# Kernel tuning notes

Measured on AMD Instinct MI355X. Metric: run time of the kernel, lower is better.

## Reference

```python
import jax, jax.numpy as jnp
import numpy as np

EMBED = 1024
HEADS = 16
HEAD_DIM = EMBED // HEADS
EPS = 1e-8


def setup_inputs() -> dict:
    key = jax.random.key(0)
    ks = jax.random.split(key, 10)
    s = 1.0 / np.sqrt(EMBED)
    return {
        "hidden_input": jax.random.normal(ks[0], (4, 2048, EMBED), dtype=jnp.float32),
        "Wq": jax.random.uniform(ks[1], (EMBED, EMBED), jnp.float32, -s, s),
        "bq": jax.random.uniform(ks[2], (EMBED,), jnp.float32, -s, s),
        "Wk": jax.random.uniform(ks[3], (EMBED, EMBED), jnp.float32, -s, s),
        "bk": jax.random.uniform(ks[4], (EMBED,), jnp.float32, -s, s),
        "Wv": jax.random.uniform(ks[5], (EMBED, EMBED), jnp.float32, -s, s),
        "bv": jax.random.uniform(ks[6], (EMBED,), jnp.float32, -s, s),
        "Wp": jax.random.uniform(ks[7], (EMBED, EMBED), jnp.float32, -s, s),
        "bp": jax.random.uniform(ks[8], (EMBED,), jnp.float32, -s, s),
        "gamma": jnp.ones((EMBED,), jnp.float32),
        "beta": jnp.zeros((EMBED,), jnp.float32),
    }


def reference(hidden_input, Wq, bq, Wk, bk, Wv, bv, Wp, bp, gamma, beta):
    n, l, e = hidden_input.shape
    h, d = HEADS, HEAD_DIM

    def split_heads(x):  # [n, l, e] -> [n, h, l, d]
        return x.reshape(n, l, h, d).transpose(0, 2, 1, 3)

    q = split_heads(hidden_input @ Wq + bq)
    k = split_heads(hidden_input @ Wk + bk)
    v = split_heads(hidden_input @ Wv + bv)

    scores = jnp.einsum("nhqd,nhkd->nhqk", q, k) / jnp.sqrt(jnp.float32(d))
    attn = jax.nn.softmax(scores, axis=-1)
    ctx = jnp.einsum("nhqk,nhkd->nhqd", attn, v)
    ctx = ctx.transpose(0, 2, 1, 3).reshape(n, l, e)

    out = ctx @ Wp + bp
    x = out + hidden_input
    mu = jnp.mean(x, axis=-1, keepdims=True)
    var = jnp.mean(jnp.square(x - mu), axis=-1, keepdims=True)
    return (x - mu) / jnp.sqrt(var + EPS) * gamma + beta
```

## Files before the change

### kernel.cpp

```cpp
#include <hip/hip_runtime.h>

#define EMBED 1024
#define SEQ   2048
#define BATCH 4
#define HEADS 16

typedef __attribute__((ext_vector_type(8))) short short8;
typedef __attribute__((ext_vector_type(4))) float floatx4;
typedef __attribute__((ext_vector_type(16))) float floatx16;

#define MFMA16(a, b, c) __builtin_amdgcn_mfma_f32_16x16x32_bf16((a), (b), (c), 0, 0, 0)
#define MFMA32(a, b, c) __builtin_amdgcn_mfma_f32_32x32x16_bf16((a), (b), (c), 0, 0, 0)
#define ATT_SCALE (0.125f * 1.44269504088896340736f)

static __device__ __forceinline__ unsigned short f2bf(float f) {
  union { float f; unsigned int u; } v; v.f = f;
  unsigned int u = v.u;
  u += 0x7fffu + ((u >> 16) & 1u);
  return (unsigned short)(u >> 16);
}

static __device__ __forceinline__ unsigned cvtpk(float lo, float hi) {
  unsigned r;
  asm("v_cvt_pk_bf16_f32 %0, %1, %2" : "=v"(r) : "v"(lo), "v"(hi));
  return r;
}

static __device__ __forceinline__ void async16(const unsigned short* g, unsigned short* l) {
  __builtin_amdgcn_global_load_lds(
      (const __attribute__((address_space(1))) void*)g,
      (__attribute__((address_space(3))) void*)l, 16, 0, 0);
}

__global__ __launch_bounds__(256) void k_prep(const float* __restrict__ hid,
                                              unsigned short* __restrict__ hidA,
                                              const float* __restrict__ Wq, const float* __restrict__ Wk,
                                              const float* __restrict__ Wv, const float* __restrict__ Wp,
                                              unsigned short* __restrict__ WT) {
  __shared__ unsigned short tile[64][65];
  const int bid = blockIdx.x, tid = threadIdx.x;
  if (bid < 4096) {
    int i = bid * 256 + tid;
    const float4* s = (const float4*)hid;
    float4 a = s[i * 2], b = s[i * 2 + 1];
    uint4 o;
    o.x = (unsigned)f2bf(a.x) | ((unsigned)f2bf(a.y) << 16);
    o.y = (unsigned)f2bf(a.z) | ((unsigned)f2bf(a.w) << 16);
    o.z = (unsigned)f2bf(b.x) | ((unsigned)f2bf(b.y) << 16);
    o.w = (unsigned)f2bf(b.z) | ((unsigned)f2bf(b.w) << 16);
    ((uint4*)hidA)[i] = o;
    return;
  }
  const int idx = bid - 4096;
  const int z = idx >> 8, rem = idx & 255;
  const float* src = (z == 0) ? Wq : (z == 1) ? Wk : (z == 2) ? Wv : Wp;
  unsigned short* dst = WT + (size_t)z * EMBED * EMBED;
  const int k0 = (rem & 15) * 64, n0 = (rem >> 4) * 64;
  for (int i = tid; i < 4096; i += 256) {
    int r = i >> 6, c = i & 63;
    tile[c][r] = f2bf(src[(size_t)(k0 + r) * EMBED + n0 + c]);
  }
  __syncthreads();
  for (int i = tid; i < 4096; i += 256) {
    int r = i >> 6, c = i & 63;
    dst[(size_t)(n0 + r) * EMBED + k0 + c] = tile[r][c];
  }
}

__global__ __launch_bounds__(256) void k_gemm_qkv(const unsigned short* __restrict__ A,
                                                  const unsigned short* __restrict__ BT,
                                                  const float* __restrict__ bq,
                                                  const float* __restrict__ bk,
                                                  const float* __restrict__ bv,
                                                  unsigned short* __restrict__ C,
                                                  unsigned short* __restrict__ VT) {
  __shared__ unsigned short Als[128 * 64];
  __shared__ unsigned short Bls[128 * 64];
  const int tid = threadIdx.x;
  const int by = blockIdx.y;
  const bool vmode = (by >= 16);
  const int arow0 = vmode ? (by - 16) * 128 : blockIdx.x * 128;
  const int brow0 = vmode ? blockIdx.x * 128 : by * 128;
  const int w = tid >> 6, lane = tid & 63, l16 = lane & 15, quad = lane >> 4;
  const int l7 = l16 & 7;
  const int wrow = (w >> 1) * 64, wcol = (w & 1) * 64;

  floatx4 acc[4][4];
#pragma unroll
  for (int i = 0; i < 4; ++i)
#pragma unroll
    for (int j = 0; j < 4; ++j) acc[i][j] = {0.f, 0.f, 0.f, 0.f};

  const int srow = tid >> 3;
  const int scol = (((tid & 7) ^ (srow & 7)) * 8);
  const unsigned short* Arow = vmode ? (BT + (size_t)2 * EMBED * EMBED) : A;
  const unsigned short* Brow = vmode ? A : BT;
  const unsigned short* Ap = Arow + (size_t)(arow0 + srow) * EMBED + scol;
  const unsigned short* Bp = Brow + (size_t)(brow0 + srow) * EMBED + scol;

  int ab[2], bb[2];
#pragma unroll
  for (int kc = 0; kc < 2; ++kc) {
    ab[kc] = (wrow + l16) * 64 + (((4 * kc + quad) ^ l7) << 3);
    bb[kc] = (wcol + l16) * 64 + (((4 * kc + quad) ^ l7) << 3);
  }

  for (int kt = 0; kt < 16; ++kt) {
    const int k0 = kt * 64;
#pragma unroll
    for (int i = 0; i < 4; ++i)
      async16(Ap + k0 + (size_t)i * 32 * EMBED, Als + i * 2048 + tid * 8);
#pragma unroll
    for (int i = 0; i < 4; ++i)
      async16(Bp + k0 + (size_t)i * 32 * EMBED, Bls + i * 2048 + tid * 8);
    __syncthreads();
    short8 af[4][2], bf[4][2];
#pragma unroll
    for (int mt = 0; mt < 4; ++mt)
#pragma unroll
      for (int kc = 0; kc < 2; ++kc)
        af[mt][kc] = *(const short8*)(Als + ab[kc] + mt * 1024);
#pragma unroll
    for (int nt = 0; nt < 4; ++nt)
#pragma unroll
      for (int kc = 0; kc < 2; ++kc)
        bf[nt][kc] = *(const short8*)(Bls + bb[kc] + nt * 1024);
#pragma unroll
    for (int kc = 0; kc < 2; ++kc)
#pragma unroll
      for (int mt = 0; mt < 4; ++mt)
#pragma unroll
        for (int nt = 0; nt < 4; ++nt)
          acc[mt][nt] = MFMA16(af[mt][kc], bf[nt][kc], acc[mt][nt]);
    __syncthreads();
  }

  if (!vmode) {
    const int n0 = brow0;
    const float* bsel = (n0 < 1024) ? bq : bk;
    const float scl = (n0 < 1024) ? ATT_SCALE : 1.0f;
    const int nb = n0 & 1023;
    float bias[4];
#pragma unroll
    for (int nt = 0; nt < 4; ++nt) bias[nt] = bsel[nb + wcol + nt * 16 + l16];
#pragma unroll
    for (int mt = 0; mt < 4; ++mt)
#pragma unroll
      for (int r = 0; r < 4; ++r) {
        int gm = arow0 + wrow + mt * 16 + quad * 4 + r;
        size_t base = (size_t)gm * 3072 + n0 + wcol;
#pragma unroll
        for (int nt = 0; nt < 4; ++nt)
          C[base + nt * 16 + l16] = f2bf((acc[mt][nt][r] + bias[nt]) * scl);
      }
  } else {
#pragma unroll
    for (int mt = 0; mt < 4; ++mt)
#pragma unroll
      for (int r = 0; r < 4; ++r) {
        const int drow = arow0 + wrow + mt * 16 + quad * 4 + r;
        const float bias = bv[drow];
        const int cg0 = brow0 + wcol;
        const int b = cg0 >> 11;
        const size_t base = ((size_t)((b * 16 + (drow >> 6)) * 64 + (drow & 63))) * SEQ
                            + (cg0 & 2047);
#pragma unroll
        for (int nt = 0; nt < 4; ++nt)
          VT[base + nt * 16 + l16] = f2bf(acc[mt][nt][r] + bias);
      }
  }
}

__global__ __launch_bounds__(256, 2) void k_attn(const unsigned short* __restrict__ QKV,
                                                 const unsigned short* __restrict__ VT,
                                                 unsigned short* __restrict__ CTX) {
  const int bh = blockIdx.x, qt = blockIdx.y;
  const int b = bh >> 4, h = bh & 15;
  const int tid = threadIdx.x;
  const int w = tid >> 6, lane = tid & 63;
  const int l32 = lane & 31, hi = lane >> 5;

  __shared__ unsigned short Kls[2][64 * 64];
  __shared__ unsigned short Vls[2][64 * 64];
  __shared__ float rsls[4][64];

  const unsigned short* Qb = QKV + (size_t)(b * SEQ + qt * 256 + w * 64) * 3072 + h * 64;
  const unsigned short* Kb = QKV + (size_t)(b * SEQ) * 3072 + 1024 + h * 64;
  const unsigned short* Vb = VT + (size_t)bh * 64 * SEQ;

  short8 qf[2][4];
#pragma unroll
  for (int qg = 0; qg < 2; ++qg)
#pragma unroll
    for (int ds = 0; ds < 4; ++ds)
      qf[qg][ds] = *(const short8*)(Qb + (size_t)(qg * 32 + l32) * 3072 + ds * 16 + hi * 8);

  floatx16 o[2][2];
  float rs[2] = {0.f, 0.f};
#pragma unroll
  for (int qg = 0; qg < 2; ++qg)
#pragma unroll
    for (int dg = 0; dg < 2; ++dg)
#pragma unroll
      for (int c = 0; c < 16; ++c) o[qg][dg][c] = 0.f;

  const int srow = tid >> 3;
  const int scol = (((tid & 7) ^ (srow & 7)) * 8);

  async16(Kb + (size_t)srow * 3072 + scol, Kls[0] + tid * 8);
  async16(Kb + (size_t)(32 + srow) * 3072 + scol, Kls[0] + 2048 + tid * 8);
  async16(Vb + (size_t)srow * SEQ + scol, Vls[0] + tid * 8);
  async16(Vb + (size_t)(32 + srow) * SEQ + scol, Vls[0] + 2048 + tid * 8);
  __syncthreads();

  int cur = 0;
  for (int kt = 0; kt < 32; ++kt) {
    if (kt < 31) {
      const int kn = (kt + 1) * 64;
      unsigned short* Kd = Kls[cur ^ 1];
      unsigned short* Vd = Vls[cur ^ 1];
      async16(Kb + (size_t)(kn + srow) * 3072 + scol, Kd + tid * 8);
      async16(Kb + (size_t)(kn + 32 + srow) * 3072 + scol, Kd + 2048 + tid * 8);
      async16(Vb + (size_t)srow * SEQ + kn + scol, Vd + tid * 8);
      async16(Vb + (size_t)(32 + srow) * SEQ + kn + scol, Vd + 2048 + tid * 8);
    }
    const unsigned short* Kc = Kls[cur];
    const unsigned short* Vc = Vls[cur];

    short8 pa[2][4];
#pragma unroll
    for (int kvg = 0; kvg < 2; ++kvg) {
      short8 kf[4];
#pragma unroll
      for (int ds = 0; ds < 4; ++ds) {
        const int row = kvg * 32 + l32;
        kf[ds] = *(const short8*)(Kc + row * 64 + (((ds * 2 + hi) ^ (row & 7)) << 3));
      }
#pragma unroll
      for (int qg = 0; qg < 2; ++qg) {
        floatx16 s;
#pragma unroll
        for (int c = 0; c < 16; ++c) s[c] = 0.f;
#pragma unroll
        for (int ds = 0; ds < 4; ++ds) s = MFMA32(kf[ds], qf[qg][ds], s);
        float p[16];
#pragma unroll
        for (int c = 0; c < 16; ++c) p[c] = __builtin_amdgcn_exp2f(s[c]);
        rs[qg] += (((p[0] + p[1]) + (p[2] + p[3])) + ((p[4] + p[5]) + (p[6] + p[7])))
                + (((p[8] + p[9]) + (p[10] + p[11])) + ((p[12] + p[13]) + (p[14] + p[15])));
#pragma unroll
        for (int half = 0; half < 2; ++half) {
          unsigned w0 = cvtpk(p[half * 8 + 0], p[half * 8 + 1]);
          unsigned w1 = cvtpk(p[half * 8 + 2], p[half * 8 + 3]);
          unsigned w2 = cvtpk(p[half * 8 + 4], p[half * 8 + 5]);
          unsigned w3 = cvtpk(p[half * 8 + 6], p[half * 8 + 7]);
          asm("v_permlane32_swap_b32 %0, %1" : "+v"(w0), "+v"(w2));
          asm("v_permlane32_swap_b32 %0, %1" : "+v"(w1), "+v"(w3));
          union { unsigned u[4]; short8 s8; } pk;
          pk.u[0] = w0; pk.u[1] = w1; pk.u[2] = w2; pk.u[3] = w3;
          pa[qg][kvg * 2 + half] = pk.s8;
        }
      }
    }

#pragma unroll
    for (int dg = 0; dg < 2; ++dg) {
      short8 vf[4];
#pragma unroll
      for (int ks = 0; ks < 4; ++ks) {
        const int row = dg * 32 + l32;
        vf[ks] = *(const short8*)(Vc + row * 64 + (((ks * 2 + hi) ^ (row & 7)) << 3));
      }
#pragma unroll
      for (int qg = 0; qg < 2; ++qg)
#pragma unroll
        for (int ks = 0; ks < 4; ++ks)
          o[qg][dg] = MFMA32(pa[qg][ks], vf[ks], o[qg][dg]);
    }

    __syncthreads();
    cur ^= 1;
  }

  rs[0] += __shfl_xor(rs[0], 32);
  rs[1] += __shfl_xor(rs[1], 32);
  if (lane < 32) {
    rsls[w][l32] = rs[0];
    rsls[w][32 + l32] = rs[1];
  }

#pragma unroll
  for (int qg = 0; qg < 2; ++qg)
#pragma unroll
    for (int j = 0; j < 16; ++j) {
      const int rl = (j & 3) + 8 * (j >> 2) + 4 * hi;
      const float inv = 1.f / rsls[w][qg * 32 + rl];
      const int gq = b * SEQ + qt * 256 + w * 64 + qg * 32 + rl;
      const size_t base = (size_t)gq * EMBED + h * 64;
#pragma unroll
      for (int dg = 0; dg < 2; ++dg)
        CTX[base + dg * 32 + l32] = f2bf(o[qg][dg][j] * inv);
    }
}

__global__ __launch_bounds__(256) void k_gemm_proj(const unsigned short* __restrict__ A,
                                                   const unsigned short* __restrict__ BT,
                                                   const float* __restrict__ bp,
                                                   const float* __restrict__ hid,
                                                   float* __restrict__ X) {
  __shared__ unsigned short Als[128 * 64];
  __shared__ unsigned short Bls[128 * 64];
  const int tid = threadIdx.x;
  const int m0 = blockIdx.x * 128, n0 = blockIdx.y * 128;
  const int w = tid >> 6, lane = tid & 63, l16 = lane & 15, quad = lane >> 4;
  const int l7 = l16 & 7;
  const int wrow = (w >> 1) * 64, wcol = (w & 1) * 64;

  floatx4 acc[4][4];
#pragma unroll
  for (int i = 0; i < 4; ++i)
#pragma unroll
    for (int j = 0; j < 4; ++j) acc[i][j] = {0.f, 0.f, 0.f, 0.f};

  const int srow = tid >> 3;
  const int scol = (((tid & 7) ^ (srow & 7)) * 8);
  const unsigned short* Ap = A + (size_t)(m0 + srow) * EMBED + scol;
  const unsigned short* Bp = BT + (size_t)(n0 + srow) * EMBED + scol;

  int ab[2], bb[2];
#pragma unroll
  for (int kc = 0; kc < 2; ++kc) {
    ab[kc] = (wrow + l16) * 64 + (((4 * kc + quad) ^ l7) << 3);
    bb[kc] = (wcol + l16) * 64 + (((4 * kc + quad) ^ l7) << 3);
  }

  for (int kt = 0; kt < 16; ++kt) {
    const int k0 = kt * 64;
#pragma unroll
    for (int i = 0; i < 4; ++i)
      async16(Ap + k0 + (size_t)i * 32 * EMBED, Als + i * 2048 + tid * 8);
#pragma unroll
    for (int i = 0; i < 4; ++i)
      async16(Bp + k0 + (size_t)i * 32 * EMBED, Bls + i * 2048 + tid * 8);
    __syncthreads();
    short8 af[4][2], bf[4][2];
#pragma unroll
    for (int mt = 0; mt < 4; ++mt)
#pragma unroll
      for (int kc = 0; kc < 2; ++kc)
        af[mt][kc] = *(const short8*)(Als + ab[kc] + mt * 1024);
#pragma unroll
    for (int nt = 0; nt < 4; ++nt)
#pragma unroll
      for (int kc = 0; kc < 2; ++kc)
        bf[nt][kc] = *(const short8*)(Bls + bb[kc] + nt * 1024);
#pragma unroll
    for (int kc = 0; kc < 2; ++kc)
#pragma unroll
      for (int mt = 0; mt < 4; ++mt)
#pragma unroll
        for (int nt = 0; nt < 4; ++nt)
          acc[mt][nt] = MFMA16(af[mt][kc], bf[nt][kc], acc[mt][nt]);
    __syncthreads();
  }

  float bias[4];
#pragma unroll
  for (int nt = 0; nt < 4; ++nt) bias[nt] = bp[n0 + wcol + nt * 16 + l16];
#pragma unroll
  for (int mt = 0; mt < 4; ++mt)
#pragma unroll
    for (int r = 0; r < 4; ++r) {
      int gm = m0 + wrow + mt * 16 + quad * 4 + r;
      size_t base = (size_t)gm * EMBED + n0 + wcol;
#pragma unroll
      for (int nt = 0; nt < 4; ++nt) {
        size_t idx = base + nt * 16 + l16;
        X[idx] = acc[mt][nt][r] + bias[nt] + hid[idx];
      }
    }
}

__global__ __launch_bounds__(256) void k_ln(float* __restrict__ x,
                                            const float* __restrict__ gamma,
                                            const float* __restrict__ beta) {
  int row = blockIdx.x, tid = threadIdx.x;
  float4* rp = (float4*)(x + (size_t)row * EMBED);
  float4 v = rp[tid];
  float s = v.x + v.y + v.z + v.w;
  float q = v.x * v.x + v.y * v.y + v.z * v.z + v.w * v.w;
#pragma unroll
  for (int off = 1; off < 64; off <<= 1) {
    s += __shfl_xor(s, off);
    q += __shfl_xor(q, off);
  }
  __shared__ float ss[4], sq[4];
  int w = tid >> 6;
  if ((tid & 63) == 0) { ss[w] = s; sq[w] = q; }
  __syncthreads();
  s = ss[0] + ss[1] + ss[2] + ss[3];
  q = sq[0] + sq[1] + sq[2] + sq[3];
  float mean = s * (1.f / 1024.f);
  float var = q * (1.f / 1024.f) - mean * mean;
  float rstd = rsqrtf(var + 1e-8f);
  float4 g = ((const float4*)gamma)[tid];
  float4 be = ((const float4*)beta)[tid];
  v.x = (v.x - mean) * rstd * g.x + be.x;
  v.y = (v.y - mean) * rstd * g.y + be.y;
  v.z = (v.z - mean) * rstd * g.z + be.z;
  v.w = (v.w - mean) * rstd * g.w + be.w;
  rp[tid] = v;
}

extern "C" void kernel_launch(void* const* d_in, const int* in_sizes, int n_in,
                              void* d_out, int out_size, void* d_ws, size_t ws_size,
                              hipStream_t stream) {
  const float* hid   = (const float*)d_in[0];
  const float* Wq    = (const float*)d_in[1];
  const float* bq    = (const float*)d_in[2];
  const float* Wk    = (const float*)d_in[3];
  const float* bk    = (const float*)d_in[4];
  const float* Wv    = (const float*)d_in[5];
  const float* bv    = (const float*)d_in[6];
  const float* Wp    = (const float*)d_in[7];
  const float* bp    = (const float*)d_in[8];
  const float* gamma = (const float*)d_in[9];
  const float* beta  = (const float*)d_in[10];
  float* out = (float*)d_out;

  char* ws = (char*)d_ws;
  unsigned short* hidA = (unsigned short*)ws;
  unsigned short* WT   = (unsigned short*)(ws + (size_t)(16 << 20));
  unsigned short* QKV  = (unsigned short*)(ws + (size_t)(24 << 20));
  unsigned short* VT   = (unsigned short*)(ws + (size_t)(72 << 20));
  unsigned short* CTX  = (unsigned short*)(ws + (size_t)(88 << 20));

  k_prep<<<5120, 256, 0, stream>>>(hid, hidA, Wq, Wk, Wv, Wp, WT);
  k_gemm_qkv<<<dim3(64, 24), 256, 0, stream>>>(hidA, WT, bq, bk, bv, QKV, VT);
  k_attn<<<dim3(64, 8), 256, 0, stream>>>(QKV, VT, CTX);
  k_gemm_proj<<<dim3(64, 8), 256, 0, stream>>>(CTX, WT + (size_t)3 * EMBED * EMBED, bp, hid, out);
  k_ln<<<8192, 256, 0, stream>>>(out, gamma, beta);
}
```

Before: 278.3 us.

## Software-pipeline QK^T one tile ahead of softmax and PV in attention

The attention loop now computes the QK^T scores for key tile kt+1 at the end of iteration kt and keeps them in registers for the next iteration's exp, pack and PV MFMAs. K and V loads are split into separate prefetch schedules: K is fetched two tiles ahead and V one tile ahead. The aim is to break the dependency between score MFMAs and the exp/convert work within an iteration so the two can overlap. The cost is 64 extra accumulator VGPRs per thread, which raises register pressure under the 256x2 launch bound.

New measurement: 278.0 us. Within noise of the previous version (-0.1%).

```diff
diff --git a/kernel.cpp b/kernel.cpp
--- a/kernel.cpp
+++ b/kernel.cpp
@@ -171,6 +171,30 @@
   }
 }
 
+static __device__ __forceinline__ void qk_step(const unsigned short* Kc,
+                                               const short8 qf[2][4],
+                                               int l32, int hi,
+                                               floatx16 S[2][2]) {
+#pragma unroll
+  for (int kvg = 0; kvg < 2; ++kvg) {
+    short8 kf[4];
+#pragma unroll
+    for (int ds = 0; ds < 4; ++ds) {
+      const int row = kvg * 32 + l32;
+      kf[ds] = *(const short8*)(Kc + row * 64 + (((ds * 2 + hi) ^ (row & 7)) << 3));
+    }
+#pragma unroll
+    for (int qg = 0; qg < 2; ++qg) {
+      floatx16 s;
+#pragma unroll
+      for (int c = 0; c < 16; ++c) s[c] = 0.f;
+#pragma unroll
+      for (int ds = 0; ds < 4; ++ds) s = MFMA32(kf[ds], qf[qg][ds], s);
+      S[kvg][qg] = s;
+    }
+  }
+}
+
 __global__ __launch_bounds__(256, 2) void k_attn(const unsigned short* __restrict__ QKV,
                                                  const unsigned short* __restrict__ VT,
                                                  unsigned short* __restrict__ CTX) {
@@ -196,6 +220,7 @@
       qf[qg][ds] = *(const short8*)(Qb + (size_t)(qg * 32 + l32) * 3072 + ds * 16 + hi * 8);
 
   floatx16 o[2][2];
+  floatx16 S[2][2];
   float rs[2] = {0.f, 0.f};
 #pragma unroll
   for (int qg = 0; qg < 2; ++qg)
@@ -211,41 +236,36 @@
   async16(Kb + (size_t)(32 + srow) * 3072 + scol, Kls[0] + 2048 + tid * 8);
   async16(Vb + (size_t)srow * SEQ + scol, Vls[0] + tid * 8);
   async16(Vb + (size_t)(32 + srow) * SEQ + scol, Vls[0] + 2048 + tid * 8);
+  async16(Kb + (size_t)(64 + srow) * 3072 + scol, Kls[1] + tid * 8);
+  async16(Kb + (size_t)(64 + 32 + srow) * 3072 + scol, Kls[1] + 2048 + tid * 8);
   __syncthreads();
 
-  int cur = 0;
+  qk_step(Kls[0], qf, l32, hi, S);
+  __syncthreads();
+
   for (int kt = 0; kt < 32; ++kt) {
+    const int cur = kt & 1;
     if (kt < 31) {
-      const int kn = (kt + 1) * 64;
-      unsigned short* Kd = Kls[cur ^ 1];
+      const int vn = (kt + 1) * 64;
       unsigned short* Vd = Vls[cur ^ 1];
+      async16(Vb + (size_t)srow * SEQ + vn + scol, Vd + tid * 8);
+      async16(Vb + (size_t)(32 + srow) * SEQ + vn + scol, Vd + 2048 + tid * 8);
+    }
+    if (kt < 30) {
+      const int kn = (kt + 2) * 64;
+      unsigned short* Kd = Kls[cur];
       async16(Kb + (size_t)(kn + srow) * 3072 + scol, Kd + tid * 8);
       async16(Kb + (size_t)(kn + 32 + srow) * 3072 + scol, Kd + 2048 + tid * 8);
-      async16(Vb + (size_t)srow * SEQ + kn + scol, Vd + tid * 8);
-      async16(Vb + (size_t)(32 + srow) * SEQ + kn + scol, Vd + 2048 + tid * 8);
-    }
-    const unsigned short* Kc = Kls[cur];
-    const unsigned short* Vc = Vls[cur];
+    }
 
     short8 pa[2][4];
 #pragma unroll
-    for (int kvg = 0; kvg < 2; ++kvg) {
-      short8 kf[4];
-#pragma unroll
-      for (int ds = 0; ds < 4; ++ds) {
-        const int row = kvg * 32 + l32;
-        kf[ds] = *(const short8*)(Kc + row * 64 + (((ds * 2 + hi) ^ (row & 7)) << 3));
-      }
+    for (int kvg = 0; kvg < 2; ++kvg)
 #pragma unroll
       for (int qg = 0; qg < 2; ++qg) {
-        floatx16 s;
-#pragma unroll
-        for (int c = 0; c < 16; ++c) s[c] = 0.f;
-#pragma unroll
-        for (int ds = 0; ds < 4; ++ds) s = MFMA32(kf[ds], qf[qg][ds], s);
         float p[16];
 #pragma unroll
-        for (int c = 0; c < 16; ++c) p[c] = __builtin_amdgcn_exp2f(s[c]);
+        for (int c = 0; c < 16; ++c) p[c] = __builtin_amdgcn_exp2f(S[kvg][qg][c]);
         rs[qg] += (((p[0] + p[1]) + (p[2] + p[3])) + ((p[4] + p[5]) + (p[6] + p[7])))
                 + (((p[8] + p[9]) + (p[10] + p[11])) + ((p[12] + p[13]) + (p[14] + p[15])));
 #pragma unroll
@@ -261,7 +281,6 @@
           pa[qg][kvg * 2 + half] = pk.s8;
         }
       }
-    }
 
 #pragma unroll
     for (int dg = 0; dg < 2; ++dg) {
@@ -269,7 +288,7 @@
 #pragma unroll
       for (int ks = 0; ks < 4; ++ks) {
         const int row = dg * 32 + l32;
-        vf[ks] = *(const short8*)(Vc + row * 64 + (((ks * 2 + hi) ^ (row & 7)) << 3));
+        vf[ks] = *(const short8*)(Vls[cur] + row * 64 + (((ks * 2 + hi) ^ (row & 7)) << 3));
       }
 #pragma unroll
       for (int qg = 0; qg < 2; ++qg)
@@ -278,8 +297,9 @@
           o[qg][dg] = MFMA32(pa[qg][ks], vf[ks], o[qg][dg]);
     }
 
+    if (kt < 31) qk_step(Kls[cur ^ 1], qf, l32, hi, S);
+
     __syncthreads();
-    cur ^= 1;
   }
 
   rs[0] += __shfl_xor(rs[0], 32);
```
